# Performance work log

Measured on AMD Instinct MI355X. Metric: run time of the kernel, lower is better.

## Reference

```python
import jax, jax.numpy as jnp
import numpy as np

N, D_IN, HID, OUT, E = 131072, 256, 1024, 1, 100


def setup_inputs() -> dict:
    key = jax.random.key(0)
    k = jax.random.split(key, 7)
    return {
        "x": jax.random.normal(k[0], (N, D_IN), dtype=jnp.float32),
        "W1": jax.random.normal(k[1], (HID, D_IN), dtype=jnp.float32) * 0.05,
        "b1": jax.random.normal(k[2], (HID,), dtype=jnp.float32) * 0.05,
        "We": jax.random.normal(k[3], (E, OUT, HID), dtype=jnp.float32) * 0.05,
        "be": jax.random.normal(k[4], (E, OUT), dtype=jnp.float32) * 0.05,
        "num": jax.random.randint(k[5], (N,), 0, E, dtype=jnp.int64),
        "c": jax.random.randint(k[6], (E,), 0, E, dtype=jnp.int64),
    }


def reference(x, W1, b1, We, be, num, c):
    # feature: Linear + ReLU  -> [N, HID]
    h = jax.nn.relu(x @ W1.T + b1)
    # per-sample expert index: c[num[i]]
    e = c[num]                                  # [N]
    Wg = We[e]                                  # [N, OUT, HID] gathered expert weights
    bg = be[e]                                  # [N, OUT]
    y = jnp.einsum('noh,nh->no', Wg, h) + bg    # per-sample expert linear
    return jax.nn.sigmoid(y)
```

## Files before the change

kernel.cpp:

```cpp
#include <hip/hip_runtime.h>
#include <stdint.h>

#define N_SAMP 131072
#define DIN    256
#define HIDN   1024
#define BROWS  128
#define NCHUNK 16

typedef __attribute__((ext_vector_type(8))) short short8;
typedef __attribute__((ext_vector_type(4))) float f32x4;

__device__ __forceinline__ unsigned short f2bf(float f) {
  unsigned u = __float_as_uint(f);
  u += 0x7fffu + ((u >> 16) & 1u);
  return (unsigned short)(u >> 16);
}

__device__ __forceinline__ short8 pack8(float4 a, float4 b) {
  short8 r;
  r[0] = (short)f2bf(a.x); r[1] = (short)f2bf(a.y);
  r[2] = (short)f2bf(a.z); r[3] = (short)f2bf(a.w);
  r[4] = (short)f2bf(b.x); r[5] = (short)f2bf(b.y);
  r[6] = (short)f2bf(b.z); r[7] = (short)f2bf(b.w);
  return r;
}

__global__ __launch_bounds__(256) void w1_to_bf16(const float* __restrict__ W1,
                                                  unsigned short* __restrict__ o) {
  int i = blockIdx.x * 256 + threadIdx.x;
  float4 f = ((const float4*)W1)[i];
  ushort4 v;
  v.x = f2bf(f.x); v.y = f2bf(f.y); v.z = f2bf(f.z); v.w = f2bf(f.w);
  ((ushort4*)o)[i] = v;
}

template <bool WBF>
__global__ __launch_bounds__(256, 2) void fused_kernel(
    const float* __restrict__ x,
    const float* __restrict__ W1f,
    const unsigned short* __restrict__ W1b,
    const float* __restrict__ b1,
    const float* __restrict__ We,
    const float* __restrict__ be,
    const int* __restrict__ num,
    const int* __restrict__ c,
    float* __restrict__ out)
{
  __shared__ unsigned short Wt[2][64 * DIN];
  __shared__ int e_sh[BROWS];

  const int tid  = threadIdx.x;
  const int lane = tid & 63;
  const int w    = tid >> 6;
  const int n    = lane & 15;
  const int quad = lane >> 4;
  const int R0   = blockIdx.x * BROWS;

  if (tid < BROWS) e_sh[tid] = c[num[R0 + tid]];

  short8 afr[2][8];
  {
    const float* xr0 = x + (size_t)(R0 + w * 32 + n) * DIN + quad * 8;
#pragma unroll
    for (int t = 0; t < 2; ++t) {
      const float* xr = xr0 + (size_t)t * 16 * DIN;
#pragma unroll
      for (int s = 0; s < 8; ++s) {
        float4 f0 = *(const float4*)(xr + s * 32);
        float4 f1 = *(const float4*)(xr + s * 32 + 4);
        afr[t][s] = pack8(f0, f1);
      }
    }
  }

  const int h2 = lane >> 5;
  const int p  = lane & 31;

  if (WBF) {
#pragma unroll
    for (int j = 0; j < 8; ++j) {
      int inst = w * 8 + j;
      int r = inst * 2 + h2;
      int kg = p ^ ((r & 7) << 2);
      const unsigned short* g = W1b + (r << 8) + (kg << 3);
      __builtin_amdgcn_global_load_lds(
          (const __attribute__((address_space(1))) unsigned int*)g,
          (__attribute__((address_space(3))) unsigned int*)(&Wt[0][0] + inst * 512),
          16, 0, 0);
    }
  } else {
#pragma unroll
    for (int j = 0; j < 8; ++j) {
      int id = tid + j * 256;
      int r = id >> 5, pp = id & 31;
      int kg = pp ^ ((r & 7) << 2);
      const float* gs = W1f + (r << 8) + (kg << 3);
      float4 f0 = *(const float4*)gs;
      float4 f1 = *(const float4*)(gs + 4);
      *(short8*)&Wt[0][r * DIN + pp * 8] = pack8(f0, f1);
    }
  }

  __syncthreads();

  int eoff[2][4];
#pragma unroll
  for (int t = 0; t < 2; ++t)
#pragma unroll
    for (int r = 0; r < 4; ++r)
      eoff[t][r] = e_sh[w * 32 + t * 16 + quad * 4 + r] * HIDN;

  float yacc[2][4] = {{0.f, 0.f, 0.f, 0.f}, {0.f, 0.f, 0.f, 0.f}};

  int buf = 0;
  for (int ch = 0; ch < NCHUNK; ++ch) {
    if (ch + 1 < NCHUNK) {
      if (WBF) {
        const unsigned short* Wg = W1b + (size_t)(ch + 1) * (64 * DIN);
        unsigned short* db = &Wt[buf ^ 1][0];
#pragma unroll
        for (int j = 0; j < 8; ++j) {
          int inst = w * 8 + j;
          int r = inst * 2 + h2;
          int kg = p ^ ((r & 7) << 2);
          const unsigned short* g = Wg + (r << 8) + (kg << 3);
          __builtin_amdgcn_global_load_lds(
              (const __attribute__((address_space(1))) unsigned int*)g,
              (__attribute__((address_space(3))) unsigned int*)(db + inst * 512),
              16, 0, 0);
        }
      } else {
        const float* Wg = W1f + (size_t)(ch + 1) * (64 * DIN);
#pragma unroll
        for (int j = 0; j < 8; ++j) {
          int id = tid + j * 256;
          int r = id >> 5, pp = id & 31;
          int kg = pp ^ ((r & 7) << 2);
          const float* gs = Wg + (r << 8) + (kg << 3);
          float4 f0 = *(const float4*)gs;
          float4 f1 = *(const float4*)(gs + 4);
          *(short8*)&Wt[buf ^ 1][r * DIN + pp * 8] = pack8(f0, f1);
        }
      }
    }

    const unsigned short* WtB = &Wt[buf][0];
    f32x4 acc[2][4];
#pragma unroll
    for (int t = 0; t < 2; ++t)
#pragma unroll
      for (int nt = 0; nt < 4; ++nt)
        acc[t][nt] = (f32x4){0.f, 0.f, 0.f, 0.f};

#pragma unroll
    for (int s = 0; s < 8; ++s) {
      const int F = (s * 4 + quad) ^ ((n & 7) << 2);
      short8 bfr[4];
#pragma unroll
      for (int nt = 0; nt < 4; ++nt)
        bfr[nt] = *(const short8*)&WtB[(nt * 16 + n) * DIN + F * 8];
#pragma unroll
      for (int t = 0; t < 2; ++t)
#pragma unroll
        for (int nt = 0; nt < 4; ++nt)
          acc[t][nt] = __builtin_amdgcn_mfma_f32_16x16x32_bf16(
              afr[t][s], bfr[nt], acc[t][nt], 0, 0, 0);
    }

#pragma unroll
    for (int nt = 0; nt < 4; ++nt) {
      int col = ch * 64 + nt * 16 + n;
      float bv = b1[col];
      const float* Wec = We + col;
#pragma unroll
      for (int t = 0; t < 2; ++t)
#pragma unroll
        for (int r = 0; r < 4; ++r) {
          float h = acc[t][nt][r] + bv;
          h = fmaxf(h, 0.f);
          yacc[t][r] = fmaf(h, Wec[eoff[t][r]], yacc[t][r]);
        }
    }

    __syncthreads();
    buf ^= 1;
  }

#pragma unroll
  for (int t = 0; t < 2; ++t)
#pragma unroll
    for (int r = 0; r < 4; ++r) {
      float v = yacc[t][r];
      v += __shfl_xor(v, 1);
      v += __shfl_xor(v, 2);
      v += __shfl_xor(v, 4);
      v += __shfl_xor(v, 8);
      yacc[t][r] = v;
    }

  if (n == 0) {
#pragma unroll
    for (int t = 0; t < 2; ++t)
#pragma unroll
      for (int r = 0; r < 4; ++r) {
        int row = R0 + w * 32 + t * 16 + quad * 4 + r;
        float yy = yacc[t][r] + be[eoff[t][r] >> 10];
        out[row] = 1.f / (1.f + __expf(-yy));
      }
  }
}

extern "C" void kernel_launch(void* const* d_in, const int* in_sizes, int n_in,
                              void* d_out, int out_size, void* d_ws, size_t ws_size,
                              hipStream_t stream) {
  const float* x   = (const float*)d_in[0];
  const float* W1  = (const float*)d_in[1];
  const float* b1  = (const float*)d_in[2];
  const float* We  = (const float*)d_in[3];
  const float* be  = (const float*)d_in[4];
  const int*   num = (const int*)d_in[5];
  const int*   c   = (const int*)d_in[6];
  float* out = (float*)d_out;

  const size_t w1bf_bytes = (size_t)HIDN * DIN * sizeof(unsigned short);
  const bool usebf = ws_size >= w1bf_bytes;
  unsigned short* w1bf = (unsigned short*)d_ws;

  if (usebf) {
    w1_to_bf16<<<dim3((HIDN * DIN / 4) / 256), dim3(256), 0, stream>>>(W1, w1bf);
    fused_kernel<true><<<dim3(N_SAMP / BROWS), dim3(256), 0, stream>>>(
        x, W1, w1bf, b1, We, be, num, c, out);
  } else {
    fused_kernel<false><<<dim3(N_SAMP / BROWS), dim3(256), 0, stream>>>(
        x, W1, w1bf, b1, We, be, num, c, out);
  }
}
```

Baseline: 260.9 us.

## Double rows per block and restructure MFMA loop to reuse W1 tiles

Each block now processes 256 rows instead of 128, so every W1 chunk staged in LDS feeds twice as many rows, halving total W1 traffic and the number of blocks. The inner loop is reordered to run per column tile, so one B fragment serves four row tiles and the accumulators stay small. Expert indices are packed into bytes to save registers, and the A-fragment loads are moved after the first W1 prefetch is issued. The cost is twice the A-fragment registers per thread, which may lower occupancy under the launch bounds of 2, and half as many blocks across the CUs.

```diff
diff --git a/kernel.cpp b/kernel.cpp
--- a/kernel.cpp
+++ b/kernel.cpp
@@ -4,8 +4,9 @@
 #define N_SAMP 131072
 #define DIN    256
 #define HIDN   1024
-#define BROWS  128
-#define NCHUNK 16
+#define BROWS  256
+#define CCOLS  64
+#define NCHUNK (HIDN / CCOLS)
 
 typedef __attribute__((ext_vector_type(8))) short short8;
 typedef __attribute__((ext_vector_type(4))) float f32x4;
@@ -46,7 +47,7 @@
     const int* __restrict__ c,
     float* __restrict__ out)
 {
-  __shared__ unsigned short Wt[2][64 * DIN];
+  __shared__ unsigned short Wt[2][CCOLS * DIN];
   __shared__ int e_sh[BROWS];
 
   const int tid  = threadIdx.x;
@@ -55,23 +56,7 @@
   const int n    = lane & 15;
   const int quad = lane >> 4;
   const int R0   = blockIdx.x * BROWS;
-
-  if (tid < BROWS) e_sh[tid] = c[num[R0 + tid]];
-
-  short8 afr[2][8];
-  {
-    const float* xr0 = x + (size_t)(R0 + w * 32 + n) * DIN + quad * 8;
-#pragma unroll
-    for (int t = 0; t < 2; ++t) {
-      const float* xr = xr0 + (size_t)t * 16 * DIN;
-#pragma unroll
-      for (int s = 0; s < 8; ++s) {
-        float4 f0 = *(const float4*)(xr + s * 32);
-        float4 f1 = *(const float4*)(xr + s * 32 + 4);
-        afr[t][s] = pack8(f0, f1);
-      }
-    }
-  }
+  const int rb   = w * 64;
 
   const int h2 = lane >> 5;
   const int p  = lane & 31;
@@ -101,22 +86,46 @@
     }
   }
 
+  e_sh[tid] = c[num[R0 + tid]];
+
+  short8 afr[4][8];
+  {
+    const float* xr0 = x + (size_t)(R0 + rb + n) * DIN + quad * 8;
+#pragma unroll
+    for (int t = 0; t < 4; ++t) {
+      const float* xr = xr0 + (size_t)t * 16 * DIN;
+#pragma unroll
+      for (int s = 0; s < 8; ++s) {
+        float4 f0 = *(const float4*)(xr + s * 32);
+        float4 f1 = *(const float4*)(xr + s * 32 + 4);
+        afr[t][s] = pack8(f0, f1);
+      }
+    }
+  }
+
   __syncthreads();
 
-  int eoff[2][4];
-#pragma unroll
-  for (int t = 0; t < 2; ++t)
+  unsigned ep[4];
+#pragma unroll
+  for (int t = 0; t < 4; ++t) {
+    unsigned v = 0;
 #pragma unroll
     for (int r = 0; r < 4; ++r)
-      eoff[t][r] = e_sh[w * 32 + t * 16 + quad * 4 + r] * HIDN;
-
-  float yacc[2][4] = {{0.f, 0.f, 0.f, 0.f}, {0.f, 0.f, 0.f, 0.f}};
+      v |= ((unsigned)e_sh[rb + t * 16 + quad * 4 + r]) << (8 * r);
+    ep[t] = v;
+  }
+
+  float yacc[4][4];
+#pragma unroll
+  for (int t = 0; t < 4; ++t)
+#pragma unroll
+    for (int r = 0; r < 4; ++r) yacc[t][r] = 0.f;
 
   int buf = 0;
   for (int ch = 0; ch < NCHUNK; ++ch) {
     if (ch + 1 < NCHUNK) {
       if (WBF) {
-        const unsigned short* Wg = W1b + (size_t)(ch + 1) * (64 * DIN);
+        const unsigned short* Wg = W1b + (size_t)(ch + 1) * (CCOLS * DIN);
         unsigned short* db = &Wt[buf ^ 1][0];
 #pragma unroll
         for (int j = 0; j < 8; ++j) {
@@ -130,7 +139,7 @@
               16, 0, 0);
         }
       } else {
-        const float* Wg = W1f + (size_t)(ch + 1) * (64 * DIN);
+        const float* Wg = W1f + (size_t)(ch + 1) * (CCOLS * DIN);
 #pragma unroll
         for (int j = 0; j < 8; ++j) {
           int id = tid + j * 256;
@@ -145,40 +154,33 @@
     }
 
     const unsigned short* WtB = &Wt[buf][0];
-    f32x4 acc[2][4];
-#pragma unroll
-    for (int t = 0; t < 2; ++t)
-#pragma unroll
-      for (int nt = 0; nt < 4; ++nt)
-        acc[t][nt] = (f32x4){0.f, 0.f, 0.f, 0.f};
-
-#pragma unroll
-    for (int s = 0; s < 8; ++s) {
-      const int F = (s * 4 + quad) ^ ((n & 7) << 2);
-      short8 bfr[4];
-#pragma unroll
-      for (int nt = 0; nt < 4; ++nt)
-        bfr[nt] = *(const short8*)&WtB[(nt * 16 + n) * DIN + F * 8];
-#pragma unroll
-      for (int t = 0; t < 2; ++t)
-#pragma unroll
-        for (int nt = 0; nt < 4; ++nt)
-          acc[t][nt] = __builtin_amdgcn_mfma_f32_16x16x32_bf16(
-              afr[t][s], bfr[nt], acc[t][nt], 0, 0, 0);
-    }
 
 #pragma unroll
     for (int nt = 0; nt < 4; ++nt) {
-      int col = ch * 64 + nt * 16 + n;
-      float bv = b1[col];
+      f32x4 acc[4];
+#pragma unroll
+      for (int t = 0; t < 4; ++t) acc[t] = (f32x4){0.f, 0.f, 0.f, 0.f};
+
+#pragma unroll
+      for (int s = 0; s < 8; ++s) {
+        const int F = (s * 4 + quad) ^ ((n & 7) << 2);
+        short8 bfr = *(const short8*)&WtB[(nt * 16 + n) * DIN + F * 8];
+#pragma unroll
+        for (int t = 0; t < 4; ++t)
+          acc[t] = __builtin_amdgcn_mfma_f32_16x16x32_bf16(
+              afr[t][s], bfr, acc[t], 0, 0, 0);
+      }
+
+      const int col = ch * CCOLS + nt * 16 + n;
+      const float bv = b1[col];
       const float* Wec = We + col;
 #pragma unroll
-      for (int t = 0; t < 2; ++t)
+      for (int t = 0; t < 4; ++t)
 #pragma unroll
         for (int r = 0; r < 4; ++r) {
-          float h = acc[t][nt][r] + bv;
-          h = fmaxf(h, 0.f);
-          yacc[t][r] = fmaf(h, Wec[eoff[t][r]], yacc[t][r]);
+          float h = fmaxf(acc[t][r] + bv, 0.f);
+          int e = (ep[t] >> (8 * r)) & 255;
+          yacc[t][r] = fmaf(h, Wec[e << 10], yacc[t][r]);
         }
     }
 
@@ -187,7 +189,7 @@
   }
 
 #pragma unroll
-  for (int t = 0; t < 2; ++t)
+  for (int t = 0; t < 4; ++t)
 #pragma unroll
     for (int r = 0; r < 4; ++r) {
       float v = yacc[t][r];
@@ -200,11 +202,12 @@
 
   if (n == 0) {
 #pragma unroll
-    for (int t = 0; t < 2; ++t)
+    for (int t = 0; t < 4; ++t)
 #pragma unroll
       for (int r = 0; r < 4; ++r) {
-        int row = R0 + w * 32 + t * 16 + quad * 4 + r;
-        float yy = yacc[t][r] + be[eoff[t][r] >> 10];
+        int row = R0 + rb + t * 16 + quad * 4 + r;
+        int e = (ep[t] >> (8 * r)) & 255;
+        float yy = yacc[t][r] + be[e];
         out[row] = 1.f / (1.f + __expf(-yy));
       }
   }
```

New measurement: 376.1 us. +44.2%, slower.
